# Performance work log

Measured on AMD Instinct MI355X. Metric: run time of the kernel, lower is better.

Reference implementation:

```python
import jax, jax.numpy as jnp
import numpy as np

B = 512      # batch per stream
L = 600      # audio length (22 chunks of 75, step 25)
DIM = 256    # model dim
H = 8        # num heads (each head is full-width, per original code)
CH = [1, DIM // 4, DIM // 2, DIM]
KS = [26, 26, 25]
EPS = 1e-5
N_CHUNKS, CHUNK, STEP = 22, 75, 25


def setup_inputs() -> dict:
    key = jax.random.key(0)
    ks = iter(jax.random.split(key, 40))
    def rn(shape, scale=0.05):
        return jax.random.normal(next(ks), shape, jnp.float32) * scale
    inp = {}
    inp["audio_vec1"] = jax.random.normal(next(ks), (B, 1, L), jnp.float32)
    inp["audio_vec2"] = jax.random.normal(next(ks), (B, 1, L), jnp.float32)
    for i in range(3):
        inp[f"conv_w{i+1}"] = rn((CH[i + 1], CH[i], KS[i]))  # OIH, torch Conv1d layout
        inp[f"conv_b{i+1}"] = rn((CH[i + 1],))
        inp[f"bn_g{i+1}"] = jnp.ones((CH[i + 1],), jnp.float32)
        inp[f"bn_b{i+1}"] = jnp.zeros((CH[i + 1],), jnp.float32)
        inp[f"bn_m{i+1}"] = rn((CH[i + 1],))
        inp[f"bn_v{i+1}"] = jnp.ones((CH[i + 1],), jnp.float32)
    # per-head Q/K/V projections (stored [H, in, out]; torch Linear is x @ W.T + b)
    inp["Wq"] = rn((H, DIM, DIM)); inp["bq"] = rn((H, DIM))
    inp["Wk"] = rn((H, DIM, DIM)); inp["bk"] = rn((H, DIM))
    inp["Wv"] = rn((H, DIM, DIM)); inp["bv"] = rn((H, DIM))
    inp["fca_w"] = rn((H * DIM, DIM)); inp["fca_b"] = rn((DIM,))
    inp["fc_w"] = rn((DIM, DIM)); inp["fc_b"] = rn((DIM,))
    return inp


def _chunks(x):
    # x: [B, 1, L] -> [B*22, 1, 75] (batched chunks, chunk-major within each example)
    idx = jnp.arange(N_CHUNKS)[:, None] * STEP + jnp.arange(CHUNK)[None, :]  # [22, 75]
    c = x[:, :, idx]                      # [B, 1, 22, 75]
    return c.transpose(0, 2, 1, 3).reshape(-1, 1, CHUNK)


def _block(x, w, b, g, bt, m, v):
    # Conv1d (valid) + BatchNorm (eval) + Swish; dropout is identity in eval.
    y = jax.lax.conv_general_dilated(
        x, w, window_strides=(1,), padding="VALID",
        dimension_numbers=("NCH", "OIH", "NCH")) + b[None, :, None]
    scale = g * jax.lax.rsqrt(v + EPS)
    y = (y - m[None, :, None]) * scale[None, :, None] + bt[None, :, None]
    return y * jax.nn.sigmoid(y)


def _forward(audio_vec1, audio_vec2,
             conv_w1, conv_b1, bn_g1, bn_b1, bn_m1, bn_v1,
             conv_w2, conv_b2, bn_g2, bn_b2, bn_m2, bn_v2,
             conv_w3, conv_b3, bn_g3, bn_b3, bn_m3, bn_v3,
             Wq, bq, Wk, bk, Wv, bv, fca_w, fca_b, fc_w, fc_b):
    # Batch both streams and all 22 chunks through one conv stack.
    X = jnp.concatenate([_chunks(audio_vec1), _chunks(audio_vec2)], axis=0)  # [2*B*22,1,75]
    X = _block(X, conv_w1, conv_b1, bn_g1, bn_b1, bn_m1, bn_v1)  # [., 64, 50]
    X = _block(X, conv_w2, conv_b2, bn_g2, bn_b2, bn_m2, bn_v2)  # [., 128, 25]
    X = _block(X, conv_w3, conv_b3, bn_g3, bn_b3, bn_m3, bn_v3)  # [., 256, 1]
    feat = X[:, :, 0].reshape(-1, N_CHUNKS, DIM)  # [2B, 22, 256]

    # Multi-head attention: 8 independent full-width heads, no 1/sqrt(d) scaling.
    Q = jnp.einsum("bse,heo->bhso", feat, Wq) + bq[None, :, None, :]
    K = jnp.einsum("bse,heo->bhso", feat, Wk) + bk[None, :, None, :]
    V = jnp.einsum("bse,heo->bhso", feat, Wv) + bv[None, :, None, :]
    A = jax.nn.softmax(jnp.einsum("bhso,bhto->bhst", Q, K), axis=-1)
    O = jnp.einsum("bhst,bhto->bhso", A, V)          # [2B, H, 22, 256]
    O = O.transpose(0, 2, 1, 3).reshape(O.shape[0], N_CHUNKS, H * DIM)
    out = O @ fca_w + fca_b                            # [2B, 22, 256]

    pooled = out.mean(axis=1)                          # [2B, 256]
    y = pooled @ fc_w + fc_b                           # [2B, 256]
    nb = audio_vec1.shape[0]
    return y[:nb], y[nb:]


def reference(audio_vec1, audio_vec2,
              conv_w1, conv_b1, bn_g1, bn_b1, bn_m1, bn_v1,
              conv_w2, conv_b2, bn_g2, bn_b2, bn_m2, bn_v2,
              conv_w3, conv_b3, bn_g3, bn_b3, bn_m3, bn_v3,
              Wq, bq, Wk, bk, Wv, bv, fca_w, fca_b, fc_w, fc_b):
    return _forward(audio_vec1, audio_vec2,
                    conv_w1, conv_b1, bn_g1, bn_b1, bn_m1, bn_v1,
                    conv_w2, conv_b2, bn_g2, bn_b2, bn_m2, bn_v2,
                    conv_w3, conv_b3, bn_g3, bn_b3, bn_m3, bn_v3,
                    Wq, bq, Wk, bk, Wv, bv, fca_w, fca_b, fc_w, fc_b)
```

## Files before the change

kernel.cpp:

```cpp
#include <hip/hip_runtime.h>
#include <hip/hip_bf16.h>
#include <math.h>

#define NSEQ 22528
#define HALFSEQ 11264

typedef __attribute__((ext_vector_type(8))) short short8;
typedef __attribute__((ext_vector_type(4))) float f32x4;
typedef __attribute__((ext_vector_type(4))) ushort ushort4v;

__device__ __forceinline__ ushort f2bf(float x) {
    __hip_bfloat16 h = __float2bfloat16(x);
    return *reinterpret_cast<ushort*>(&h);
}
__device__ __forceinline__ float bf2f(ushort u) {
    unsigned v = ((unsigned)u) << 16;
    return *reinterpret_cast<float*>(&v);
}
__device__ __forceinline__ unsigned pkbf(float lo, float hi) {
    unsigned r;
    asm("v_cvt_pk_bf16_f32 %0, %1, %2" : "=v"(r) : "v"(lo), "v"(hi));
    return r;
}
__device__ __forceinline__ float fsilu(float y) {
    float e = __expf(-y);
    return y * __builtin_amdgcn_rcpf(1.f + e);
}

__global__ __launch_bounds__(256) void k_prep_misc(
    const float* __restrict__ Wk, float* __restrict__ WkT,
    const float* __restrict__ bq, float* __restrict__ kb,
    const float* __restrict__ bv, const float* __restrict__ fca_w,
    const float* __restrict__ fca_b, float* __restrict__ bvc,
    const float* __restrict__ Wv, float* __restrict__ F,
    const float* __restrict__ b3c, const float* __restrict__ g3,
    const float* __restrict__ be3, const float* __restrict__ m3,
    const float* __restrict__ v3, float* __restrict__ sh3)
{
    __shared__ float smem[16 * 256];
    const int bid = blockIdx.x;
    const int tid = threadIdx.x;

    if (bid < 2048) {
        int idx = bid * 256 + tid;
        int b = idx >> 16;
        int rem = idx & 65535;
        int c = rem >> 8;
        int r = rem & 255;
        WkT[idx] = Wk[(size_t)(b * 256 + r) * 256 + c];
    } else if (bid < 2056) {
        int h = bid - 2048;
        smem[tid] = bq[h * 256 + tid];
        __syncthreads();
        const float* wk = Wk + (size_t)(h * 256 + tid) * 256;
        float a = 0.f;
        for (int o = 0; o < 256; ++o) a += wk[o] * smem[o];
        kb[h * 256 + tid] = a;
    } else if (bid < 2057) {
        for (int i = tid; i < 2048; i += 256) smem[i] = bv[i];
        __syncthreads();
        float acc = fca_b[tid];
        for (int k = 0; k < 2048; ++k) acc += smem[k] * fca_w[(size_t)k * 256 + tid];
        bvc[tid] = acc;
    } else if (bid < 2185) {
        int lb = bid - 2057;
        int h = lb >> 4;
        int e0 = (lb & 15) * 16;
        for (int idx = tid; idx < 4096; idx += 256) {
            int r = idx >> 8;
            int c = idx & 255;
            smem[r * 256 + c] = Wv[(size_t)h * 65536 + (e0 + r) * 256 + c];
        }
        __syncthreads();
        float acc[16];
        #pragma unroll
        for (int r = 0; r < 16; ++r) acc[r] = 0.f;
        for (int o = 0; o < 256; ++o) {
            float w = fca_w[(size_t)(h * 256 + o) * 256 + tid];
            #pragma unroll
            for (int r = 0; r < 16; ++r) acc[r] += smem[r * 256 + o] * w;
        }
        #pragma unroll
        for (int r = 0; r < 16; ++r)
            F[(size_t)(h * 256 + e0 + r) * 256 + tid] = acc[r];
    } else {
        float A = g3[tid] * rsqrtf(v3[tid] + 1e-5f);
        sh3[tid] = (b3c[tid] - m3[tid]) * A + be3[tid];
    }
}

__global__ __launch_bounds__(256) void k_prep_w2t(
    const float* __restrict__ w2, ushort* __restrict__ w2f,
    const float* __restrict__ g2, const float* __restrict__ v2)
{
    __shared__ float tile[13312];
    const int mt = blockIdx.x >> 1;
    const int ich = blockIdx.x & 1;
    const int tid = threadIdx.x;
    for (int idx = tid; idx < 13312; idx += 256) {
        int oc16 = idx / 832;
        int rem = idx - oc16 * 832;
        tile[idx] = w2[(size_t)(mt * 16 + oc16) * 1664 + ich * 832 + rem];
    }
    __syncthreads();
    for (int wi = tid; wi < 26 * 512; wi += 256) {
        int t = wi >> 9;
        int li = wi & 511;
        int lane = li >> 3;
        int j = li & 7;
        int oc16 = lane & 15;
        int il = ((lane >> 4) << 3) + j;
        int oc = mt * 16 + oc16;
        float A = g2[oc] * rsqrtf(v2[oc] + 1e-5f);
        w2f[(size_t)(((2 * t + ich) * 8 + mt) << 9) + li] = f2bf(tile[oc16 * 832 + il * 26 + t] * A);
    }
}

__global__ __launch_bounds__(256) void k_prep_w3t(
    const float* __restrict__ w3, ushort* __restrict__ w3f,
    const float* __restrict__ g3, const float* __restrict__ v3)
{
    __shared__ float tile[12800];
    const int mt = blockIdx.x >> 2;
    const int icb = blockIdx.x & 3;
    const int tid = threadIdx.x;
    for (int idx = tid; idx < 12800; idx += 256) {
        int oc16 = idx / 800;
        int rem = idx - oc16 * 800;
        tile[idx] = w3[(size_t)(mt * 16 + oc16) * 3200 + icb * 800 + rem];
    }
    __syncthreads();
    for (int wi = tid; wi < 25 * 512; wi += 256) {
        int pos = wi >> 9;
        int li = wi & 511;
        int lane = li >> 3;
        int j = li & 7;
        int oc16 = lane & 15;
        int il = ((lane >> 4) << 3) + j;
        int oc = mt * 16 + oc16;
        float A = g3[oc] * rsqrtf(v3[oc] + 1e-5f);
        w3f[(size_t)(((pos * 4 + icb) * 16 + mt) << 9) + li] = f2bf(tile[oc16 * 800 + il * 25 + pos] * A);
    }
}

__global__ __launch_bounds__(256) void k_prep_attn_m(
    const float* __restrict__ Wq, const float* __restrict__ WkT,
    float* __restrict__ M)
{
    const int h = blockIdx.x >> 4;
    const int e0 = (blockIdx.x & 15) * 16;
    const int tid = threadIdx.x;
    __shared__ float sq[16][256];
    for (int idx = tid; idx < 4096; idx += 256) {
        int r = idx >> 8;
        int c = idx & 255;
        sq[r][c] = Wq[(size_t)(h * 256 + e0 + r) * 256 + c];
    }
    __syncthreads();
    float acc[16];
    #pragma unroll
    for (int r = 0; r < 16; ++r) acc[r] = 0.f;
    const float* wkt = WkT + (size_t)h * 65536 + tid;
    for (int o = 0; o < 256; ++o) {
        float wk = wkt[o * 256];
        #pragma unroll
        for (int r = 0; r < 16; ++r) acc[r] += sq[r][o] * wk;
    }
    #pragma unroll
    for (int r = 0; r < 16; ++r)
        M[(size_t)(h * 256 + e0 + r) * 256 + tid] = acc[r];
}

__global__ void k_prep_mfrag(const float* __restrict__ M, ushort* __restrict__ Mfrag,
                             const float* __restrict__ kb, ushort* __restrict__ kbf) {
    int bid = blockIdx.x;
    int tid = threadIdx.x;
    if (bid < 2048) {
        int idx = bid * 256 + tid;
        int j = idx & 7;
        int lane = (idx >> 3) & 63;
        int mt = (idx >> 9) & 15;
        int kt = (idx >> 13) & 7;
        int h = idx >> 16;
        int e = kt * 32 + ((lane >> 4) << 3) + j;
        int o = mt * 16 + (lane & 15);
        Mfrag[idx] = f2bf(M[(size_t)(h * 256 + e) * 256 + o]);
    } else {
        int idx = (bid - 2048) * 256 + tid;
        int j = idx & 7;
        int lane = (idx >> 3) & 63;
        int kt = idx >> 9;
        int h = lane & 15;
        int e = kt * 32 + ((lane >> 4) << 3) + j;
        kbf[idx] = (h < 8) ? f2bf(kb[h * 256 + e]) : (ushort)0;
    }
}

__global__ __launch_bounds__(512, 4) void k_conv(
    const float* __restrict__ av1, const float* __restrict__ av2,
    const float* __restrict__ w1,
    const float* __restrict__ b1c, const float* __restrict__ g1,
    const float* __restrict__ be1, const float* __restrict__ m1, const float* __restrict__ v1,
    const ushort* __restrict__ w2f,
    const float* __restrict__ b2c, const float* __restrict__ g2,
    const float* __restrict__ be2, const float* __restrict__ m2, const float* __restrict__ v2,
    ushort* __restrict__ a2f, int seqoff)
{
    __shared__ ushort s_a1[8 * 3200];
    __shared__ ushort s_w1f[2048];
    __shared__ ushort s_xb[8][80];
    __shared__ float s_sh1[64], s_sh2[128];

    const int tid = threadIdx.x;
    const int lane = tid & 63;
    const int w = tid >> 6;
    const int l15 = lane & 15;
    const int grp = lane >> 4;
    const int lseq0 = blockIdx.x * 8;
    const int gseq0 = seqoff + lseq0;

    for (int idx = tid; idx < 640; idx += 512) {
        int s = idx / 80;
        int i = idx - s * 80;
        int seq = gseq0 + s;
        const float* src;
        if (seq < HALFSEQ) { int b = seq / 22; int n = seq - b * 22; src = av1 + b * 600 + n * 25; }
        else { int q = seq - HALFSEQ; int b = q / 22; int n = q - b * 22; src = av2 + b * 600 + n * 25; }
        s_xb[s][i] = f2bf((i < 75) ? src[i] : 0.f);
    }
    for (int idx = tid; idx < 2048; idx += 512) {
        int j = idx & 7;
        int ln = (idx >> 3) & 63;
        int mt = idx >> 9;
        int oc = mt * 16 + (ln & 15);
        int k = ((ln >> 4) << 3) + j;
        float A = g1[oc] * rsqrtf(v1[oc] + 1e-5f);
        s_w1f[idx] = (k < 26) ? f2bf(w1[oc * 26 + k] * A) : (ushort)0;
    }
    if (tid < 64) {
        float A = g1[tid] * rsqrtf(v1[tid] + 1e-5f);
        s_sh1[tid] = (b1c[tid] - m1[tid]) * A + be1[tid];
    }
    if (tid >= 128 && tid < 256) {
        int o = tid - 128;
        float A = g2[o] * rsqrtf(v2[o] + 1e-5f);
        s_sh2[o] = (b2c[o] - m2[o]) * A + be2[o];
    }
    __syncthreads();

    {
        short8 a1f[4];
        #pragma unroll
        for (int mt = 0; mt < 4; ++mt)
            a1f[mt] = *(const short8*)(s_w1f + mt * 512 + lane * 8);

        for (int nt = w; nt < 25; nt += 8) {
            int n = nt * 16 + l15;
            int s = n / 50;
            int p = n - s * 50;
            short8 bf;
            #pragma unroll
            for (int j = 0; j < 8; ++j) {
                int t = grp * 8 + j;
                bf[j] = (t < 26) ? (short)s_xb[s][p + t] : (short)0;
            }
            #pragma unroll
            for (int mt = 0; mt < 4; ++mt) {
                f32x4 acc1 = (f32x4){0.f, 0.f, 0.f, 0.f};
                acc1 = __builtin_amdgcn_mfma_f32_16x16x32_bf16(a1f[mt], bf, acc1, 0, 0, 0);
                int oc0 = mt * 16 + grp * 4;
                int icb = oc0 >> 3;
                int boff = s * 6400 + icb * 800 + p * 16 + (oc0 & 7) * 2;
                float y0 = fsilu(acc1[0] + s_sh1[oc0 + 0]);
                float y1 = fsilu(acc1[1] + s_sh1[oc0 + 1]);
                float y2 = fsilu(acc1[2] + s_sh1[oc0 + 2]);
                float y3 = fsilu(acc1[3] + s_sh1[oc0 + 3]);
                uint2 u;
                u.x = pkbf(y0, y1);
                u.y = pkbf(y2, y3);
                *(uint2*)((char*)s_a1 + boff) = u;
            }
        }
    }
    __syncthreads();

    {
        const int mset = w & 3;
        const int nset = w >> 2;
        const int NT = nset ? 6 : 7;

        int vaddr[7];
        #pragma unroll
        for (int ni = 0; ni < 7; ++ni) {
            int nt = nset * 7 + ni;
            int n = nt * 16 + l15;
            int s = n / 25; if (s > 7) s = 7;
            int p = n - s * 25; if (p > 24) p = 24;
            vaddr[ni] = s * 6400 + grp * 800 + p * 16;
        }

        f32x4 acc[2][7];
        #pragma unroll
        for (int mi = 0; mi < 2; ++mi)
            #pragma unroll
            for (int ni = 0; ni < 7; ++ni)
                acc[mi][ni] = (f32x4){0.f, 0.f, 0.f, 0.f};

        const ushort* wpt = w2f + (size_t)(mset * 2) * 512 + lane * 8;
        short8 afA0 = *(const short8*)(wpt);
        short8 afA1 = *(const short8*)(wpt + 512);
        short8 afB0 = *(const short8*)(wpt + 4096);
        short8 afB1 = *(const short8*)(wpt + 4096 + 512);

        for (int t = 0; t < 26; ++t) {
            #pragma unroll
            for (int ni = 0; ni < 7; ++ni) {
                if (ni >= NT) break;
                short8 bf = *(const short8*)((const char*)s_a1 + vaddr[ni]);
                acc[0][ni] = __builtin_amdgcn_mfma_f32_16x16x32_bf16(afA0, bf, acc[0][ni], 0, 0, 0);
                acc[1][ni] = __builtin_amdgcn_mfma_f32_16x16x32_bf16(afA1, bf, acc[1][ni], 0, 0, 0);
            }
            if (t < 25) {
                afA0 = *(const short8*)(wpt + 8192);
                afA1 = *(const short8*)(wpt + 8192 + 512);
            }
            #pragma unroll
            for (int ni = 0; ni < 7; ++ni) {
                if (ni >= NT) break;
                short8 bf = *(const short8*)((const char*)s_a1 + vaddr[ni] + 3200);
                acc[0][ni] = __builtin_amdgcn_mfma_f32_16x16x32_bf16(afB0, bf, acc[0][ni], 0, 0, 0);
                acc[1][ni] = __builtin_amdgcn_mfma_f32_16x16x32_bf16(afB1, bf, acc[1][ni], 0, 0, 0);
            }
            if (t < 25) {
                afB0 = *(const short8*)(wpt + 12288);
                afB1 = *(const short8*)(wpt + 12288 + 512);
                wpt += 8192;
            }
            #pragma unroll
            for (int ni = 0; ni < 7; ++ni) vaddr[ni] += 16;
        }

        #pragma unroll
        for (int mi = 0; mi < 2; ++mi) {
            const int ocb = mset * 32 + mi * 16 + grp * 4;
            const int grp_dst = (ocb >> 3) & 3;
            const int jb = ocb & 7;
            const int kthi = ocb >> 5;
            #pragma unroll
            for (int ni = 0; ni < 7; ++ni) {
                if (ni >= NT) break;
                int n = (nset * 7 + ni) * 16 + l15;
                if (n < 200) {
                    int s = n / 25;
                    int p = n - s * 25;
                    int seq = lseq0 + s;
                    int kt3 = p * 4 + kthi;
                    float y0 = fsilu(acc[mi][ni][0] + s_sh2[ocb + 0]);
                    float y1 = fsilu(acc[mi][ni][1] + s_sh2[ocb + 1]);
                    float y2 = fsilu(acc[mi][ni][2] + s_sh2[ocb + 2]);
                    float y3 = fsilu(acc[mi][ni][3] + s_sh2[ocb + 3]);
                    uint2 u;
                    u.x = pkbf(y0, y1);
                    u.y = pkbf(y2, y3);
                    *(uint2*)(a2f + (((size_t)(seq >> 4) * 100 + kt3) << 9)
                              + ((seq & 15) + 16 * grp_dst) * 8 + jb) = u;
                }
            }
        }
    }
}

__global__ __launch_bounds__(256) void k_conv3(
    const ushort* __restrict__ a2f, const ushort* __restrict__ w3f,
    const float* __restrict__ sh3,
    float* __restrict__ feat, int seqoff)
{
    const int tid = threadIdx.x;
    const int lane = tid & 63;
    const int wv = tid >> 6;
    const int l15 = lane & 15;
    const int grp = lane >> 4;
    const int lseq0 = blockIdx.x * 64;

    f32x4 acc3[4][4];
    #pragma unroll
    for (int mi = 0; mi < 4; ++mi)
        #pragma unroll
        for (int nt = 0; nt < 4; ++nt)
            acc3[mi][nt] = (f32x4){0.f, 0.f, 0.f, 0.f};

    const ushort* bp = a2f + ((size_t)(lseq0 >> 4) * 100) * 512 + lane * 8;
    const ushort* ap = w3f + (size_t)(wv * 4) * 512 + lane * 8;

    for (int kt = 0; kt < 100; ++kt) {
        short8 bf[4];
        #pragma unroll
        for (int nt = 0; nt < 4; ++nt)
            bf[nt] = *(const short8*)(bp + (size_t)(nt * 100 + kt) * 512);
        #pragma unroll
        for (int mi = 0; mi < 4; ++mi) {
            short8 af = *(const short8*)(ap + (size_t)kt * 8192 + mi * 512);
            #pragma unroll
            for (int nt = 0; nt < 4; ++nt)
                acc3[mi][nt] = __builtin_amdgcn_mfma_f32_16x16x32_bf16(af, bf[nt], acc3[mi][nt], 0, 0, 0);
        }
    }

    #pragma unroll
    for (int nt = 0; nt < 4; ++nt) {
        int gseq = seqoff + lseq0 + nt * 16 + l15;
        #pragma unroll
        for (int mi = 0; mi < 4; ++mi) {
            int oc = wv * 64 + mi * 16 + grp * 4;
            float4 o4;
            #pragma unroll
            for (int r = 0; r < 4; ++r)
                ((float*)&o4)[r] = fsilu(acc3[mi][nt][r] + sh3[oc + r]);
            *(float4*)(feat + (size_t)gseq * 256 + oc) = o4;
        }
    }
}

__global__ __launch_bounds__(512, 2) void k_attn_f(
    const float* __restrict__ feat, const ushort* __restrict__ Mfrag,
    const ushort* __restrict__ kbf, float* __restrict__ fbar_all)
{
    const int g0 = blockIdx.x * 2;
    const int tid = threadIdx.x;
    const int lane = tid & 63;
    const int wv = tid >> 6;
    const int l15 = lane & 15;
    const int grp = lane >> 4;

    __shared__ __align__(16) ushort sfb[2 * 32 * 256];
    __shared__ __align__(16) ushort sG[2 * 32 * 256];
    __shared__ float sS[2 * 528];
    __shared__ float sbet[2 * 192];
    __shared__ float sab[2 * 24];

    char* const sfbb = (char*)sfb;
    char* const sGb = (char*)sG;

    for (int idx = tid; idx < 16384; idx += 512) {
        int gg = idx >> 13;
        int s = (idx >> 8) & 31;
        int e = idx & 255;
        float f = (s < 22) ? feat[(size_t)(g0 + gg) * 5632 + s * 256 + e] : 0.f;
        int byte = gg * 16384 + s * 512 + ((e * 2) ^ ((s & 7) << 4));
        *(ushort*)(sfbb + byte) = f2bf(f);
    }
    __syncthreads();

    if (wv < 4) {
        int gg = wv >> 1;
        int rowb = (wv & 1) * 16;
        int rA = rowb + l15;
        f32x4 acc = (f32x4){0.f, 0.f, 0.f, 0.f};
        for (int kt = 0; kt < 8; ++kt) {
            int e0b = (kt * 32 + grp * 8) * 2;
            short8 af = *(const short8*)(sfbb + gg * 16384 + rA * 512 + (e0b ^ ((rA & 7) << 4)));
            short8 bf = *(const short8*)(kbf + kt * 512 + lane * 8);
            acc = __builtin_amdgcn_mfma_f32_16x16x32_bf16(af, bf, acc, 0, 0, 0);
        }
        #pragma unroll
        for (int r = 0; r < 4; ++r) {
            int t = rowb + grp * 4 + r;
            int h = l15;
            if (t < 22 && h < 8) sbet[gg * 192 + h * 24 + t] = acc[r];
        }
    }
    __syncthreads();

    for (int h = 0; h < 8; ++h) {
        {
            f32x4 accg[4][2];
            #pragma unroll
            for (int mt = 0; mt < 4; ++mt)
                #pragma unroll
                for (int fi = 0; fi < 2; ++fi)
                    accg[mt][fi] = (f32x4){0.f, 0.f, 0.f, 0.f};

            const ushort* mfb = Mfrag + (size_t)h * 65536;
            for (int kt = 0; kt < 8; ++kt) {
                int e0b = (kt * 32 + grp * 8) * 2;
                short8 af[4];
                #pragma unroll
                for (int mt = 0; mt < 4; ++mt) {
                    int gg = mt >> 1;
                    int rA = (mt & 1) * 16 + l15;
                    af[mt] = *(const short8*)(sfbb + gg * 16384 + rA * 512 + (e0b ^ ((rA & 7) << 4)));
                }
                #pragma unroll
                for (int fi = 0; fi < 2; ++fi) {
                    int ft = wv * 2 + fi;
                    short8 bfm = *(const short8*)(mfb + (size_t)((kt * 16 + ft) << 9) + lane * 8);
                    #pragma unroll
                    for (int mt = 0; mt < 4; ++mt)
                        accg[mt][fi] = __builtin_amdgcn_mfma_f32_16x16x32_bf16(af[mt], bfm, accg[mt][fi], 0, 0, 0);
                }
            }
            #pragma unroll
            for (int mt = 0; mt < 4; ++mt) {
                int gg = mt >> 1;
                #pragma unroll
                for (int fi = 0; fi < 2; ++fi) {
                    int f = (wv * 2 + fi) * 16 + l15;
                    #pragma unroll
                    for (int r = 0; r < 4; ++r) {
                        int s = (mt & 1) * 16 + grp * 4 + r;
                        if (s < 22) {
                            int byte = gg * 16384 + s * 512 + ((f * 2) ^ ((s & 7) << 4));
                            *(ushort*)(sGb + byte) = f2bf(accg[mt][fi][r]);
                        }
                    }
                }
            }
        }
        __syncthreads();

        {
            int gg = wv >> 2;
            int mt2 = (wv >> 1) & 1;
            int nt2 = wv & 1;
            f32x4 sacc = (f32x4){0.f, 0.f, 0.f, 0.f};
            int sA = mt2 * 16 + l15;
            int tB = nt2 * 16 + l15;
            for (int kt = 0; kt < 8; ++kt) {
                int f0b = (kt * 32 + grp * 8) * 2;
                short8 ga = *(const short8*)(sGb + gg * 16384 + sA * 512 + (f0b ^ ((sA & 7) << 4)));
                short8 fb = *(const short8*)(sfbb + gg * 16384 + tB * 512 + (f0b ^ ((tB & 7) << 4)));
                sacc = __builtin_amdgcn_mfma_f32_16x16x32_bf16(ga, fb, sacc, 0, 0, 0);
            }
            #pragma unroll
            for (int r = 0; r < 4; ++r) {
                int s = mt2 * 16 + grp * 4 + r;
                int t = nt2 * 16 + l15;
                if (s < 22 && t < 22)
                    sS[gg * 528 + s * 24 + t] = sacc[r] + sbet[gg * 192 + h * 24 + t];
            }
        }
        __syncthreads();

        if (tid < 44) {
            int gg = tid >= 22;
            int s = tid - gg * 22;
            float* row = sS + gg * 528 + s * 24;
            float mx = -1e30f;
            #pragma unroll
            for (int t = 0; t < 22; ++t) mx = fmaxf(mx, row[t]);
            float ex[22];
            float sum = 0.f;
            #pragma unroll
            for (int t = 0; t < 22; ++t) { float e2 = __expf(row[t] - mx); ex[t] = e2; sum += e2; }
            float inv = 1.f / sum;
            #pragma unroll
            for (int t = 0; t < 22; ++t) row[t] = ex[t] * inv;
        }
        __syncthreads();
        if (tid < 44) {
            int gg = tid >= 22;
            int t = tid - gg * 22;
            float a = 0.f;
            #pragma unroll
            for (int s = 0; s < 22; ++s) a += sS[gg * 528 + s * 24 + t];
            sab[gg * 24 + t] = a * (1.f / 22.f);
        }
        __syncthreads();

        {
            int gg = tid >> 8;
            int e = tid & 255;
            int e2b = e * 2;
            float a = 0.f;
            #pragma unroll
            for (int t = 0; t < 22; ++t) {
                ushort u = *(ushort*)(sfbb + gg * 16384 + t * 512 + (e2b ^ ((t & 7) << 4)));
                a += sab[gg * 24 + t] * bf2f(u);
            }
            fbar_all[((size_t)(g0 + gg) * 8 + h) * 256 + e] = a;
        }
        __syncthreads();
    }
}

__global__ __launch_bounds__(256) void k_pool(
    const float* __restrict__ fbar_all, const float* __restrict__ F,
    const float* __restrict__ bvc,
    const float* __restrict__ fc_w, const float* __restrict__ fc_b,
    float* __restrict__ out)
{
    const int g0 = blockIdx.x * 4;
    const int tid = threadIdx.x;
    __shared__ __align__(16) float sfb[4 * 2048];
    __shared__ __align__(16) float sp[4 * 256];
    for (int idx = tid; idx < 8192; idx += 256)
        sfb[idx] = fbar_all[(size_t)g0 * 8 * 256 + idx];
    __syncthreads();

    float p[4];
    float bb = bvc[tid];
    #pragma unroll
    for (int j = 0; j < 4; ++j) p[j] = bb;
    for (int k = 0; k < 2048; k += 4) {
        float f0 = F[(size_t)(k + 0) * 256 + tid];
        float f1 = F[(size_t)(k + 1) * 256 + tid];
        float f2 = F[(size_t)(k + 2) * 256 + tid];
        float f3 = F[(size_t)(k + 3) * 256 + tid];
        #pragma unroll
        for (int j = 0; j < 4; ++j) {
            float4 v = *(const float4*)(sfb + j * 2048 + k);
            p[j] += v.x * f0 + v.y * f1 + v.z * f2 + v.w * f3;
        }
    }
    #pragma unroll
    for (int j = 0; j < 4; ++j) sp[j * 256 + tid] = p[j];
    __syncthreads();

    float y[4];
    float fb = fc_b[tid];
    #pragma unroll
    for (int j = 0; j < 4; ++j) y[j] = fb;
    for (int e = 0; e < 256; ++e) {
        float w = fc_w[(size_t)e * 256 + tid];
        #pragma unroll
        for (int j = 0; j < 4; ++j) y[j] += sp[j * 256 + e] * w;
    }
    #pragma unroll
    for (int j = 0; j < 4; ++j)
        out[(size_t)(g0 + j) * 256 + tid] = y[j];
}

extern "C" void kernel_launch(void* const* d_in, const int* in_sizes, int n_in,
                              void* d_out, int out_size, void* d_ws, size_t ws_size,
                              hipStream_t stream) {
    (void)in_sizes; (void)n_in; (void)out_size;

    const float* av1   = (const float*)d_in[0];
    const float* av2   = (const float*)d_in[1];
    const float* w1    = (const float*)d_in[2];
    const float* b1c   = (const float*)d_in[3];
    const float* g1    = (const float*)d_in[4];
    const float* be1   = (const float*)d_in[5];
    const float* m1    = (const float*)d_in[6];
    const float* v1    = (const float*)d_in[7];
    const float* w2    = (const float*)d_in[8];
    const float* b2c   = (const float*)d_in[9];
    const float* g2    = (const float*)d_in[10];
    const float* be2   = (const float*)d_in[11];
    const float* m2    = (const float*)d_in[12];
    const float* v2    = (const float*)d_in[13];
    const float* w3    = (const float*)d_in[14];
    const float* b3c   = (const float*)d_in[15];
    const float* g3    = (const float*)d_in[16];
    const float* be3   = (const float*)d_in[17];
    const float* m3    = (const float*)d_in[18];
    const float* v3    = (const float*)d_in[19];
    const float* Wq    = (const float*)d_in[20];
    const float* bq    = (const float*)d_in[21];
    const float* Wk    = (const float*)d_in[22];
    const float* bk    = (const float*)d_in[23];
    const float* Wv    = (const float*)d_in[24];
    const float* bv    = (const float*)d_in[25];
    const float* fca_w = (const float*)d_in[26];
    const float* fca_b = (const float*)d_in[27];
    const float* fc_w  = (const float*)d_in[28];
    const float* fc_b  = (const float*)d_in[29];
    (void)bk;

    float* ws = (float*)d_ws;
    float* feat = ws;
    float* Mm   = feat + 5767168;
    float* WkT  = Mm + 524288;
    float* kb   = WkT + 524288;
    float* bvc  = kb + 2048;
    float* F    = bvc + 256;
    float* fbar = F + 524288;
    float* sh3  = fbar + 2097152;
    ushort* w2f = (ushort*)(sh3 + 256);
    ushort* w3f = w2f + 212992;
    ushort* mfr = w3f + 819200;
    ushort* kbf = mfr + 524288;
    ushort* region = kbf + 4096;

    size_t base_bytes = (size_t)((char*)region - (char*)d_ws);
    size_t budget = (ws_size > base_bytes + 4096) ? (ws_size - base_bytes - 4096) : 0;
    int ncA = 16;
    const int cand[5] = {1, 2, 4, 8, 16};
    for (int i = 0; i < 5; ++i) { if ((size_t)144179200 / cand[i] <= budget) { ncA = cand[i]; break; } }
    const int seqsA = NSEQ / ncA;

    k_prep_misc<<<2186, 256, 0, stream>>>(Wk, WkT, bq, kb, bv, fca_w, fca_b, bvc, Wv, F,
                                          b3c, g3, be3, m3, v3, sh3);
    k_prep_w2t<<<16, 256, 0, stream>>>(w2, w2f, g2, v2);
    k_prep_w3t<<<64, 256, 0, stream>>>(w3, w3f, g3, v3);
    k_prep_attn_m<<<128, 256, 0, stream>>>(Wq, WkT, Mm);
    k_prep_mfrag<<<2064, 256, 0, stream>>>(Mm, mfr, kb, kbf);

    ushort* a2f = region;
    for (int c = 0; c < ncA; ++c) {
        int seqoff = c * seqsA;
        k_conv<<<seqsA / 8, 512, 0, stream>>>(av1, av2,
            w1, b1c, g1, be1, m1, v1,
            w2f, b2c, g2, be2, m2, v2,
            a2f, seqoff);
        k_conv3<<<seqsA / 64, 256, 0, stream>>>(a2f, w3f, sh3, feat, seqoff);
    }

    k_attn_f<<<512, 512, 0, stream>>>(feat, mfr, kbf, fbar);
    k_pool<<<256, 256, 0, stream>>>(fbar, F, bvc, fc_w, fc_b, (float*)d_out);
}
```

Before: 555.6 us.

## Fuse Wq·WkT prep into MFMA kernel, pad conv LDS, widen conv3 blocks

Replaces the Wk transpose, the scalar Wq·Wk^T product and the fragment-packing kernel with one MFMA-based kernel that writes bf16 Mfrag directly. This removes two launches and the fp32 M/WkT intermediates. It also pads the per-sequence LDS stride in k_conv (6400 to 6416), likely to avoid bank conflicts. k_conv3 now runs 512 threads per block, with each wave covering 32 output channels instead of 64, for more parallelism and lower register pressure. The trade-off is that the A-fragment loads for conv3 are split across more waves, so the B fragments are loaded redundantly by more waves.

```diff
diff --git a/kernel.cpp b/kernel.cpp
--- a/kernel.cpp
+++ b/kernel.cpp
@@ -8,6 +8,7 @@
 typedef __attribute__((ext_vector_type(8))) short short8;
 typedef __attribute__((ext_vector_type(4))) float f32x4;
 typedef __attribute__((ext_vector_type(4))) ushort ushort4v;
+typedef __attribute__((ext_vector_type(4))) unsigned uint4v;
 
 __device__ __forceinline__ ushort f2bf(float x) {
     __hip_bfloat16 h = __float2bfloat16(x);
@@ -28,7 +29,7 @@
 }
 
 __global__ __launch_bounds__(256) void k_prep_misc(
-    const float* __restrict__ Wk, float* __restrict__ WkT,
+    const float* __restrict__ Wk,
     const float* __restrict__ bq, float* __restrict__ kb,
     const float* __restrict__ bv, const float* __restrict__ fca_w,
     const float* __restrict__ fca_b, float* __restrict__ bvc,
@@ -41,29 +42,22 @@
     const int bid = blockIdx.x;
     const int tid = threadIdx.x;
 
-    if (bid < 2048) {
-        int idx = bid * 256 + tid;
-        int b = idx >> 16;
-        int rem = idx & 65535;
-        int c = rem >> 8;
-        int r = rem & 255;
-        WkT[idx] = Wk[(size_t)(b * 256 + r) * 256 + c];
-    } else if (bid < 2056) {
-        int h = bid - 2048;
+    if (bid < 8) {
+        int h = bid;
         smem[tid] = bq[h * 256 + tid];
         __syncthreads();
         const float* wk = Wk + (size_t)(h * 256 + tid) * 256;
         float a = 0.f;
         for (int o = 0; o < 256; ++o) a += wk[o] * smem[o];
         kb[h * 256 + tid] = a;
-    } else if (bid < 2057) {
+    } else if (bid < 9) {
         for (int i = tid; i < 2048; i += 256) smem[i] = bv[i];
         __syncthreads();
         float acc = fca_b[tid];
         for (int k = 0; k < 2048; ++k) acc += smem[k] * fca_w[(size_t)k * 256 + tid];
         bvc[tid] = acc;
-    } else if (bid < 2185) {
-        int lb = bid - 2057;
+    } else if (bid < 137) {
+        int lb = bid - 9;
         int h = lb >> 4;
         int e0 = (lb & 15) * 16;
         for (int idx = tid; idx < 4096; idx += 256) {
@@ -86,6 +80,68 @@
     } else {
         float A = g3[tid] * rsqrtf(v3[tid] + 1e-5f);
         sh3[tid] = (b3c[tid] - m3[tid]) * A + be3[tid];
+    }
+}
+
+__global__ __launch_bounds__(256) void k_prep_qk(
+    const float* __restrict__ Wq, const float* __restrict__ Wk,
+    const float* __restrict__ kb,
+    ushort* __restrict__ Mfrag, ushort* __restrict__ kbf)
+{
+    const int bid = blockIdx.x;
+    const int tid = threadIdx.x;
+    if (bid >= 8) {
+        int idx = (bid - 8) * 256 + tid;
+        int j = idx & 7;
+        int lane = (idx >> 3) & 63;
+        int kt = idx >> 9;
+        int h = lane & 15;
+        int e = kt * 32 + ((lane >> 4) << 3) + j;
+        kbf[idx] = (h < 8) ? f2bf(kb[h * 256 + e]) : (ushort)0;
+        return;
+    }
+    const int h = bid;
+    const int lane = tid & 63;
+    const int wv = tid >> 6;
+    const int l15 = lane & 15;
+    const int grp = lane >> 4;
+    const float* WqH = Wq + (size_t)h * 65536;
+    const float* WkH = Wk + (size_t)h * 65536;
+
+    for (int fi = 0; fi < 4; ++fi) {
+        int ft = wv * 4 + fi;
+        short8 bfr[8];
+        #pragma unroll
+        for (int kt2 = 0; kt2 < 8; ++kt2) {
+            const float* src = WkH + (size_t)(ft * 16 + l15) * 256 + kt2 * 32 + grp * 8;
+            float4 a = *(const float4*)(src);
+            float4 b = *(const float4*)(src + 4);
+            uint4v t;
+            t[0] = pkbf(a.x, a.y); t[1] = pkbf(a.z, a.w);
+            t[2] = pkbf(b.x, b.y); t[3] = pkbf(b.z, b.w);
+            bfr[kt2] = *(short8*)&t;
+        }
+        for (int mt = 0; mt < 16; ++mt) {
+            f32x4 acc = (f32x4){0.f, 0.f, 0.f, 0.f};
+            #pragma unroll
+            for (int kt2 = 0; kt2 < 8; ++kt2) {
+                const float* src = WqH + (size_t)(mt * 16 + l15) * 256 + kt2 * 32 + grp * 8;
+                float4 a = *(const float4*)(src);
+                float4 b = *(const float4*)(src + 4);
+                uint4v t;
+                t[0] = pkbf(a.x, a.y); t[1] = pkbf(a.z, a.w);
+                t[2] = pkbf(b.x, b.y); t[3] = pkbf(b.z, b.w);
+                short8 af = *(short8*)&t;
+                acc = __builtin_amdgcn_mfma_f32_16x16x32_bf16(af, bfr[kt2], acc, 0, 0, 0);
+            }
+            int ktt = mt >> 1;
+            int lane_t = l15 + 16 * ((mt & 1) * 2 + (grp >> 1));
+            int j0 = (grp & 1) * 4;
+            uint2 u;
+            u.x = pkbf(acc[0], acc[1]);
+            u.y = pkbf(acc[2], acc[3]);
+            *(uint2*)(Mfrag + (size_t)h * 65536 + (ktt * 16 + ft) * 512 + lane_t * 8 + j0) = u;
+        }
     }
 }
 
@@ -143,59 +199,6 @@
     }
 }
 
-__global__ __launch_bounds__(256) void k_prep_attn_m(
-    const float* __restrict__ Wq, const float* __restrict__ WkT,
-    float* __restrict__ M)
-{
-    const int h = blockIdx.x >> 4;
-    const int e0 = (blockIdx.x & 15) * 16;
-    const int tid = threadIdx.x;
-    __shared__ float sq[16][256];
-    for (int idx = tid; idx < 4096; idx += 256) {
-        int r = idx >> 8;
-        int c = idx & 255;
-        sq[r][c] = Wq[(size_t)(h * 256 + e0 + r) * 256 + c];
-    }
-    __syncthreads();
-    float acc[16];
-    #pragma unroll
-    for (int r = 0; r < 16; ++r) acc[r] = 0.f;
-    const float* wkt = WkT + (size_t)h * 65536 + tid;
-    for (int o = 0; o < 256; ++o) {
-        float wk = wkt[o * 256];
-        #pragma unroll
-        for (int r = 0; r < 16; ++r) acc[r] += sq[r][o] * wk;
-    }
-    #pragma unroll
-    for (int r = 0; r < 16; ++r)
-        M[(size_t)(h * 256 + e0 + r) * 256 + tid] = acc[r];
-}
-
-__global__ void k_prep_mfrag(const float* __restrict__ M, ushort* __restrict__ Mfrag,
-                             const float* __restrict__ kb, ushort* __restrict__ kbf) {
-    int bid = blockIdx.x;
-    int tid = threadIdx.x;
-    if (bid < 2048) {
-        int idx = bid * 256 + tid;
-        int j = idx & 7;
-        int lane = (idx >> 3) & 63;
-        int mt = (idx >> 9) & 15;
-        int kt = (idx >> 13) & 7;
-        int h = idx >> 16;
-        int e = kt * 32 + ((lane >> 4) << 3) + j;
-        int o = mt * 16 + (lane & 15);
-        Mfrag[idx] = f2bf(M[(size_t)(h * 256 + e) * 256 + o]);
-    } else {
-        int idx = (bid - 2048) * 256 + tid;
-        int j = idx & 7;
-        int lane = (idx >> 3) & 63;
-        int kt = idx >> 9;
-        int h = lane & 15;
-        int e = kt * 32 + ((lane >> 4) << 3) + j;
-        kbf[idx] = (h < 8) ? f2bf(kb[h * 256 + e]) : (ushort)0;
-    }
-}
-
 __global__ __launch_bounds__(512, 4) void k_conv(
     const float* __restrict__ av1, const float* __restrict__ av2,
     const float* __restrict__ w1,
@@ -206,7 +209,7 @@
     const float* __restrict__ be2, const float* __restrict__ m2, const float* __restrict__ v2,
     ushort* __restrict__ a2f, int seqoff)
 {
-    __shared__ ushort s_a1[8 * 3200];
+    __shared__ ushort s_a1[8 * 3208];
     __shared__ ushort s_w1f[2048];
     __shared__ ushort s_xb[8][80];
     __shared__ float s_sh1[64], s_sh2[128];
@@ -270,7 +273,7 @@
                 acc1 = __builtin_amdgcn_mfma_f32_16x16x32_bf16(a1f[mt], bf, acc1, 0, 0, 0);
                 int oc0 = mt * 16 + grp * 4;
                 int icb = oc0 >> 3;
-                int boff = s * 6400 + icb * 800 + p * 16 + (oc0 & 7) * 2;
+                int boff = s * 6416 + icb * 800 + p * 16 + (oc0 & 7) * 2;
                 float y0 = fsilu(acc1[0] + s_sh1[oc0 + 0]);
                 float y1 = fsilu(acc1[1] + s_sh1[oc0 + 1]);
                 float y2 = fsilu(acc1[2] + s_sh1[oc0 + 2]);
@@ -296,7 +299,7 @@
             int n = nt * 16 + l15;
             int s = n / 25; if (s > 7) s = 7;
             int p = n - s * 25; if (p > 24) p = 24;
-            vaddr[ni] = s * 6400 + grp * 800 + p * 16;
+            vaddr[ni] = s * 6416 + grp * 800 + p * 16;
         }
 
         f32x4 acc[2][7];
@@ -370,7 +373,7 @@
     }
 }
 
-__global__ __launch_bounds__(256) void k_conv3(
+__global__ __launch_bounds__(512) void k_conv3(
     const ushort* __restrict__ a2f, const ushort* __restrict__ w3f,
     const float* __restrict__ sh3,
     float* __restrict__ feat, int seqoff)
@@ -382,15 +385,15 @@
     const int grp = lane >> 4;
     const int lseq0 = blockIdx.x * 64;
 
-    f32x4 acc3[4][4];
+    f32x4 acc3[2][4];
     #pragma unroll
-    for (int mi = 0; mi < 4; ++mi)
+    for (int mi = 0; mi < 2; ++mi)
         #pragma unroll
         for (int nt = 0; nt < 4; ++nt)
             acc3[mi][nt] = (f32x4){0.f, 0.f, 0.f, 0.f};
 
     const ushort* bp = a2f + ((size_t)(lseq0 >> 4) * 100) * 512 + lane * 8;
-    const ushort* ap = w3f + (size_t)(wv * 4) * 512 + lane * 8;
+    const ushort* ap = w3f + (size_t)(wv * 2) * 512 + lane * 8;
 
     for (int kt = 0; kt < 100; ++kt) {
         short8 bf[4];
@@ -398,7 +401,7 @@
         for (int nt = 0; nt < 4; ++nt)
             bf[nt] = *(const short8*)(bp + (size_t)(nt * 100 + kt) * 512);
         #pragma unroll
-        for (int mi = 0; mi < 4; ++mi) {
+        for (int mi = 0; mi < 2; ++mi) {
             short8 af = *(const short8*)(ap + (size_t)kt * 8192 + mi * 512);
             #pragma unroll
             for (int nt = 0; nt < 4; ++nt)
@@ -410,8 +413,8 @@
     for (int nt = 0; nt < 4; ++nt) {
         int gseq = seqoff + lseq0 + nt * 16 + l15;
         #pragma unroll
-        for (int mi = 0; mi < 4; ++mi) {
-            int oc = wv * 64 + mi * 16 + grp * 4;
+        for (int mi = 0; mi < 2; ++mi) {
+            int oc = (wv * 2 + mi) * 16 + grp * 4;
             float4 o4;
             #pragma unroll
             for (int r = 0; r < 4; ++r)
@@ -669,9 +672,7 @@
 
     float* ws = (float*)d_ws;
     float* feat = ws;
-    float* Mm   = feat + 5767168;
-    float* WkT  = Mm + 524288;
-    float* kb   = WkT + 524288;
+    float* kb   = feat + 5767168;
     float* bvc  = kb + 2048;
     float* F    = bvc + 256;
     float* fbar = F + 524288;
@@ -689,12 +690,11 @@
     for (int i = 0; i < 5; ++i) { if ((size_t)144179200 / cand[i] <= budget) { ncA = cand[i]; break; } }
     const int seqsA = NSEQ / ncA;
 
-    k_prep_misc<<<2186, 256, 0, stream>>>(Wk, WkT, bq, kb, bv, fca_w, fca_b, bvc, Wv, F,
-                                          b3c, g3, be3, m3, v3, sh3);
+    k_prep_misc<<<138, 256, 0, stream>>>(Wk, bq, kb, bv, fca_w, fca_b, bvc, Wv, F,
+                                         b3c, g3, be3, m3, v3, sh3);
+    k_prep_qk<<<24, 256, 0, stream>>>(Wq, Wk, kb, mfr, kbf);
     k_prep_w2t<<<16, 256, 0, stream>>>(w2, w2f, g2, v2);
     k_prep_w3t<<<64, 256, 0, stream>>>(w3, w3f, g3, v3);
-    k_prep_attn_m<<<128, 256, 0, stream>>>(Wq, WkT, Mm);
-    k_prep_mfrag<<<2064, 256, 0, stream>>>(Mm, mfr, kb, kbf);
 
     ushort* a2f = region;
     for (int c = 0; c < ncA; ++c) {
@@ -703,7 +703,7 @@
             w1, b1c, g1, be1, m1, v1,
             w2f, b2c, g2, be2, m2, v2,
             a2f, seqoff);
-        k_conv3<<<seqsA / 64, 256, 0, stream>>>(a2f, w3f, sh3, feat, seqoff);
+        k_conv3<<<seqsA / 64, 512, 0, stream>>>(a2f, w3f, sh3, feat, seqoff);
     }
 
     k_attn_f<<<512, 512, 0, stream>>>(feat, mfr, kbf, fbar);
```

After: 647.2 us. 16.5% more time.
